# Kernel optimization log

Hardware: AMD Instinct MI355X
Metric: run time of the kernel (lower is better)

The kernel has to match this reference:

```python
import jax, jax.numpy as jnp
import numpy as np

IN_DIM = 256
MEM_DIM = 256
DEPTH = 18                    # complete binary tree
N = 2 ** DEPTH - 1            # 262143 nodes; children of i are 2i+1, 2i+2; node 0 is root


def _glorot(k, shape):
    lim = float(np.sqrt(6.0 / (shape[0] + shape[1])))
    return jax.random.uniform(k, shape, jnp.float32, -lim, lim)


def setup_inputs() -> dict:
    key = jax.random.key(0)
    ks = jax.random.split(key, 6)
    inputs = jax.random.normal(ks[0], (N, IN_DIM), jnp.float32)
    Wioux = _glorot(ks[1], (3 * MEM_DIM, IN_DIM))
    bioux = jnp.zeros((3 * MEM_DIM,), jnp.float32)
    Wiouh = _glorot(ks[2], (3 * MEM_DIM, MEM_DIM))
    Wfx = _glorot(ks[3], (MEM_DIM, IN_DIM))
    bfx = jnp.zeros((MEM_DIM,), jnp.float32)
    Wfh = _glorot(ks[4], (MEM_DIM, MEM_DIM))
    fb = jnp.ones((MEM_DIM,), jnp.float32)
    return {"inputs": inputs, "Wioux": Wioux, "bioux": bioux, "Wiouh": Wiouh,
            "Wfx": Wfx, "bfx": bfx, "Wfh": Wfh, "fb": fb}


def reference(inputs, Wioux, bioux, Wiouh, Wfx, bfx, Wfh, fb):
    # Child-Sum TreeLSTM over a complete binary tree, level-wise batched (bottom-up).
    n, _ = inputs.shape
    m = fb.shape[0]
    depth = int(np.log2(n + 1))
    # Input projections for all nodes at once (same math as per-node ioux/fx).
    xiou = inputs @ Wioux.T + bioux          # [N, 3m]
    xf = inputs @ Wfx.T + bfx                # [N, m]
    h_all = jnp.zeros((n, m), inputs.dtype)
    c_all = jnp.zeros((n, m), inputs.dtype)
    for d in range(depth - 1, -1, -1):
        s, e = 2 ** d - 1, 2 ** (d + 1) - 1   # nodes at level d
        if d == depth - 1:
            # Leaves: zero child state -> iouh/fh contribute 0, fc sums to 0.
            i, o, u = jnp.split(xiou[s:e], 3, axis=1)
            i, o, u = jax.nn.sigmoid(i), jax.nn.sigmoid(o), jnp.tanh(u)
            c = i * u
        else:
            node = jnp.arange(s, e)
            ch = jnp.stack([2 * node + 1, 2 * node + 2], axis=1)   # [L, 2]
            ch_h = h_all[ch]                                       # [L, 2, m]
            ch_c = c_all[ch]                                       # [L, 2, m]
            iou = xiou[s:e] + ch_h.sum(axis=1) @ Wiouh.T           # child-sum
            i, o, u = jnp.split(iou, 3, axis=1)
            i, o, u = jax.nn.sigmoid(i), jax.nn.sigmoid(o), jnp.tanh(u)
            f = jax.nn.sigmoid(jnp.einsum('lkm,nm->lkn', ch_h, Wfh)
                               + xf[s:e][:, None, :] + fb)         # per-child forget gate
            c = i * u + (f * ch_c).sum(axis=1)
        h = o * jnp.tanh(c)
        h_all = h_all.at[s:e].set(h)
        c_all = c_all.at[s:e].set(c)
    # (root h, root c, all node hidden states) as in the torch forward
    return h_all[0], c_all[0], h_all
```

## Files before the change

kernel.cpp:

```cpp
#include <hip/hip_runtime.h>


typedef __attribute__((ext_vector_type(8))) short bf16x8;
typedef __attribute__((ext_vector_type(8))) unsigned short us8;
typedef __attribute__((ext_vector_type(4))) float f32x4;
typedef __attribute__((ext_vector_type(4))) float f4;

#define MFMA16(A, B, C) __builtin_amdgcn_mfma_f32_16x16x32_bf16(A, B, C, 0, 0, 0)

__device__ __forceinline__ unsigned short f2b(float f) {
  unsigned int u = __builtin_bit_cast(unsigned int, f);
  u = u + 0x7FFFu + ((u >> 16) & 1u);
  return (unsigned short)(u >> 16);
}
__device__ __forceinline__ float bf2f(unsigned short u) {
  unsigned int v = (unsigned int)u << 16;
  return __builtin_bit_cast(float, v);
}
__device__ __forceinline__ us8 pack8(f4 a, f4 b) {
  us8 r;
  r[0] = f2b(a[0]); r[1] = f2b(a[1]); r[2] = f2b(a[2]); r[3] = f2b(a[3]);
  r[4] = f2b(b[0]); r[5] = f2b(b[1]); r[6] = f2b(b[2]); r[7] = f2b(b[3]);
  return r;
}
__device__ __forceinline__ float sigm(float x) { return 1.0f / (1.0f + __expf(-x)); }
__device__ __forceinline__ float tanh_f(float x) { return 2.0f / (1.0f + __expf(-2.0f * x)) - 1.0f; }

__global__ void pack_w(const float* __restrict__ a,
                       const float* __restrict__ b,
                       const float* __restrict__ c,
                       const float* __restrict__ d,
                       unsigned short* __restrict__ out) {
  int i = blockIdx.x * blockDim.x + threadIdx.x;
  const int A = 768 * 256;
  const int B = A + 768 * 256;
  const int C = B + 256 * 256;
  float v;
  if (i < A)      v = a[i];
  else if (i < B) v = b[i - A];
  else if (i < C) v = c[i - B];
  else            v = d[i - C];
  out[i] = f2b(v);
}

__global__ void conv_x(const float* __restrict__ x, unsigned short* __restrict__ xb, int n32) {
  int i = blockIdx.x * blockDim.x + threadIdx.x;
  if (i >= n32) return;
  const int n = i >> 5, g = i & 31;
  f4 a = __builtin_nontemporal_load((const f4*)(x + (size_t)n * 256 + g * 8));
  f4 b = __builtin_nontemporal_load((const f4*)(x + (size_t)n * 256 + g * 8 + 4));
  const int d = 31 - __clz(n + 1);
  const int r = n - ((1 << d) - 1);
  const size_t base = (size_t)((d < 4) ? d * 16 : 48 + (1 << d)) * 256;
  const size_t off = base + ((size_t)((r >> 4) * 8 + (g >> 2)) * 16 + (r & 15)) * 32
                     + (g & 3) * 8;
  __builtin_nontemporal_store(pack8(a, b), (us8*)(xb + off));
}

template<int LEAF>
__global__ __launch_bounds__(512) __attribute__((amdgpu_waves_per_eu(3, 4)))
void level_k(
    const unsigned short* __restrict__ xlv,
    const unsigned short* __restrict__ wb,
    const float* __restrict__ bioux,
    const float* __restrict__ bfx,
    const float* __restrict__ fb,
    float* __restrict__ h_all,
    const unsigned short* __restrict__ hs_r,
    const unsigned short* __restrict__ hbe_r,
    const unsigned int* __restrict__ cp_r,
    unsigned short* __restrict__ hs_w,
    unsigned short* __restrict__ hbe_w,
    unsigned int* __restrict__ cp_w,
    float* __restrict__ out0,
    int s, int L, int T16, int root, int lns)
{
  extern __shared__ unsigned short W[];

  const int tid    = threadIdx.x;
  const int NS     = 1 << lns;
  const int cg     = blockIdx.x >> lns;
  const int stripe = blockIdx.x & (NS - 1);

  const int NP = LEAF ? 3 : 8;
  #pragma unroll 1
  for (int c = tid; c < NP * 512; c += 512) {
    const int p   = c >> 9;
    const int q   = c & 511;
    const int kc  = q >> 6;
    const int kg  = (q >> 4) & 3;
    const int col = q & 15;
    const int po = (p < 3) ? p * 65536
                 : (p < 6) ? 196608 + (p - 3) * 65536
                 : (p == 6) ? 393216 : 458752;
    us8 v = *(const us8*)(wb + po + (size_t)(cg * 16 + col) * 256 + kc * 32 + kg * 8);
    *(us8*)(W + p * 4096 + ((kc * 4 + kg) * 16 + col) * 8) = v;
  }
  __syncthreads();

  const int lane = tid & 63;
  const int wv   = tid >> 6;
  const int lm   = lane & 15;
  const int kgl  = lane >> 4;
  const int colc = cg * 16 + lm;

  const unsigned short* LW = W + kgl * 128 + lm * 8;

  const int kcw = colc >> 5;
  const int kgw = (colc >> 3) & 3;
  const int ew  = colc & 7;

  const float bi_ = bioux[colc];
  const float bo_ = bioux[256 + colc];
  const float bu_ = bioux[512 + colc];
  const float bf_ = LEAF ? 0.f : (bfx[colc] + fb[colc]);

  const int Tper = (T16 + NS - 1) >> lns;
  const int t0   = stripe * Tper;
  const int tE   = (t0 + Tper < T16) ? (t0 + Tper) : T16;

  for (int t = t0 + wv; t < tE; t += 8) {
    const int tb16  = t * 16;
    const int drow0 = tb16 + kgl * 4;
    const size_t abase = (size_t)t * 4096 + lm * 32 + kgl * 8;
    const unsigned short* xr = xlv + abase;
    const f32x4 z4 = {0.f, 0.f, 0.f, 0.f};

    if (!LEAF) {
      const unsigned short* hbr = hbe_r + abase;
      const unsigned short* hsr = hs_r  + abase;

      unsigned int cpv[4];
      #pragma unroll
      for (int r = 0; r < 4; ++r)
        cpv[r] = cp_r[(size_t)t * 4096 + cg * 256 + r * 64 + kgl * 16 + lm];

      f32x4 xf = z4, f1h = z4, ai = z4, ao = z4, au = z4, fs = z4;
      #pragma unroll 4
      for (int kc = 0; kc < 8; ++kc) {
        bf16x8 ax = *(const bf16x8*)(xr  + kc * 512);
        bf16x8 a1 = *(const bf16x8*)(hbr + kc * 512);
        bf16x8 ah = *(const bf16x8*)(hsr + kc * 512);
        bf16x8 b6 = *(const bf16x8*)(LW + 6 * 4096 + kc * 512);
        bf16x8 b0 = *(const bf16x8*)(LW + 0 * 4096 + kc * 512);
        bf16x8 b1 = *(const bf16x8*)(LW + 1 * 4096 + kc * 512);
        bf16x8 b2 = *(const bf16x8*)(LW + 2 * 4096 + kc * 512);
        bf16x8 b7 = *(const bf16x8*)(LW + 7 * 4096 + kc * 512);
        bf16x8 b3 = *(const bf16x8*)(LW + 3 * 4096 + kc * 512);
        bf16x8 b4 = *(const bf16x8*)(LW + 4 * 4096 + kc * 512);
        bf16x8 b5 = *(const bf16x8*)(LW + 5 * 4096 + kc * 512);
        xf  = MFMA16(ax, b6, xf);
        ai  = MFMA16(ax, b0, ai);
        ao  = MFMA16(ax, b1, ao);
        au  = MFMA16(ax, b2, au);
        f1h = MFMA16(a1, b7, f1h);
        ai  = MFMA16(ah, b3, ai);
        ao  = MFMA16(ah, b4, ao);
        au  = MFMA16(ah, b5, au);
        fs  = MFMA16(ah, b7, fs);
      }

      float hv4[4], cv4[4];
      #pragma unroll
      for (int r = 0; r < 4; ++r) {
        const float i_ = sigm(ai[r] + bi_);
        const float u_ = tanh_f(au[r] + bu_);
        const float o_ = sigm(ao[r] + bo_);
        const float f1 = sigm(xf[r] + f1h[r] + bf_);
        const float f2 = sigm(xf[r] + fs[r] - f1h[r] + bf_);
        const float c1 = bf2f((unsigned short)(cpv[r] & 0xffffu));
        const float c2 = bf2f((unsigned short)(cpv[r] >> 16));
        const float c_ = i_ * u_ + f1 * c1 + f2 * c2;
        const float h_ = o_ * tanh_f(c_);
        cv4[r] = c_; hv4[r] = h_;
        const int j = drow0 + r;
        if (j < L)
          __builtin_nontemporal_store(h_, h_all + (size_t)(s + j) * 256 + colc);
      }
      if (root) {
        if (drow0 == 0) { out0[colc] = hv4[0]; out0[256 + colc] = cv4[0]; }
      } else {
        #pragma unroll
        for (int rp = 0; rp < 2; ++rp) {
          const int j0 = drow0 + rp * 2;
          if (j0 + 1 < L) {
            const int pp = j0 >> 1;
            const int q  = pp & 15;
            const size_t toff = ((size_t)((pp >> 4) * 8 + kcw) * 16 + q) * 32
                                + kgw * 8 + ew;
            hs_w [toff] = f2b(hv4[rp*2] + hv4[rp*2+1]);
            hbe_w[toff] = f2b(hv4[rp*2]);
            cp_w [(size_t)(pp >> 4) * 4096 + cg * 256 + (q & 3) * 64
                  + (q >> 2) * 16 + lm] =
                (unsigned int)f2b(cv4[rp*2]) | ((unsigned int)f2b(cv4[rp*2+1]) << 16);
          }
        }
      }
    } else {
      f32x4 ai = z4, ao = z4, au = z4;
      #pragma unroll 4
      for (int kc = 0; kc < 8; ++kc) {
        bf16x8 ax = *(const bf16x8*)(xr + kc * 512);
        bf16x8 b0 = *(const bf16x8*)(LW + 0 * 4096 + kc * 512);
        bf16x8 b1 = *(const bf16x8*)(LW + 1 * 4096 + kc * 512);
        bf16x8 b2 = *(const bf16x8*)(LW + 2 * 4096 + kc * 512);
        ai = MFMA16(ax, b0, ai);
        ao = MFMA16(ax, b1, ao);
        au = MFMA16(ax, b2, au);
      }
      float hv4[4], cv4[4];
      #pragma unroll
      for (int r = 0; r < 4; ++r) {
        const float i_ = sigm(ai[r] + bi_);
        const float u_ = tanh_f(au[r] + bu_);
        const float o_ = sigm(ao[r] + bo_);
        const float c_ = i_ * u_;
        const float h_ = o_ * tanh_f(c_);
        cv4[r] = c_; hv4[r] = h_;
        __builtin_nontemporal_store(h_, h_all + (size_t)(s + drow0 + r) * 256 + colc);
      }
      #pragma unroll
      for (int rp = 0; rp < 2; ++rp) {
        const int pp = (drow0 + rp * 2) >> 1;
        const int q  = pp & 15;
        const size_t toff = ((size_t)((pp >> 4) * 8 + kcw) * 16 + q) * 32
                            + kgw * 8 + ew;
        hs_w [toff] = f2b(hv4[rp*2] + hv4[rp*2+1]);
        hbe_w[toff] = f2b(hv4[rp*2]);
        cp_w [(size_t)(pp >> 4) * 4096 + cg * 256 + (q & 3) * 64
              + (q >> 2) * 16 + lm] =
            (unsigned int)f2b(cv4[rp*2]) | ((unsigned int)f2b(cv4[rp*2+1]) << 16);
      }
    }
  }
}

extern "C" void kernel_launch(void* const* d_in, const int* in_sizes, int n_in,
                              void* d_out, int out_size, void* d_ws, size_t ws_size,
                              hipStream_t stream) {
  const float* inputs = (const float*)d_in[0];
  const float* Wioux  = (const float*)d_in[1];
  const float* bioux  = (const float*)d_in[2];
  const float* Wiouh  = (const float*)d_in[3];
  const float* Wfx    = (const float*)d_in[4];
  const float* bfx    = (const float*)d_in[5];
  const float* Wfh    = (const float*)d_in[6];
  const float* fb     = (const float*)d_in[7];

  const int N = in_sizes[0] / 256;
  int depth = 0;
  while (((1 << depth) - 1) < N) ++depth;

  float* out   = (float*)d_out;
  float* h_all = out + 512;

  static bool attr_done = false;
  if (!attr_done) {
    hipFuncSetAttribute((const void*)level_k<0>,
                        hipFuncAttributeMaxDynamicSharedMemorySize, 8 * 8192);
    hipFuncSetAttribute((const void*)level_k<1>,
                        hipFuncAttributeMaxDynamicSharedMemorySize, 3 * 8192);
    attr_done = true;
  }

  char* p = (char*)d_ws;
  unsigned short* hs0  = (unsigned short*)p; p += (size_t)65536 * 256 * 2;
  unsigned short* hbe0 = (unsigned short*)p; p += (size_t)65536 * 256 * 2;
  unsigned int*   cp0  = (unsigned int*)p;   p += (size_t)65536 * 256 * 4;
  unsigned short* hs1  = (unsigned short*)p; p += (size_t)32768 * 256 * 2;
  unsigned short* hbe1 = (unsigned short*)p; p += (size_t)32768 * 256 * 2;
  unsigned int*   cp1  = (unsigned int*)p;   p += (size_t)32768 * 256 * 4;
  unsigned short* xb   = (unsigned short*)p; p += (size_t)(N + 64) * 256 * 2;
  unsigned short* wb   = (unsigned short*)p;

  pack_w<<<2048, 256, 0, stream>>>(Wioux, Wiouh, Wfx, Wfh, wb);
  {
    const int n32 = N * 32;
    conv_x<<<(n32 + 255) / 256, 256, 0, stream>>>(inputs, xb, n32);
  }

  for (int d = depth - 1; d >= 0; --d) {
    const int L = 1 << d;
    const int s = L - 1;
    const int T16 = (L + 15) / 16;
    const size_t Pb = (size_t)((d < 4) ? d * 16 : 48 + (1 << d)) * 256;
    int lg = 0; while ((1 << (lg + 1)) <= T16) ++lg;
    int lns = lg - 3; if (lns < 0) lns = 0; if (lns > 5) lns = 5;
    const int rp_ = d & 1, wp_ = (d - 1) & 1;
    const unsigned short* hs_r  = rp_ ? hs1 : hs0;
    const unsigned short* hbe_r = rp_ ? hbe1 : hbe0;
    const unsigned int*   cp_r  = rp_ ? cp1 : cp0;
    unsigned short* hs_w  = wp_ ? hs1 : hs0;
    unsigned short* hbe_w = wp_ ? hbe1 : hbe0;
    unsigned int*   cp_w  = wp_ ? cp1 : cp0;
    if (d == depth - 1) {
      level_k<1><<<16 * 64, 512, 3 * 8192, stream>>>(
          xb + Pb, wb, bioux, bfx, fb, h_all,
          hs_r, hbe_r, cp_r, hs_w, hbe_w, cp_w, out, s, L, T16, 0, 6);
    } else {
      level_k<0><<<16 << lns, 512, 8 * 8192, stream>>>(
          xb + Pb, wb, bioux, bfx, fb, h_all,
          hs_r, hbe_r, cp_r, hs_w, hbe_w, cp_w, out, s, L, T16, (d == 0) ? 1 : 0, lns);
    }
  }
}
```

Measured before the change: 681.5 us.

## Process two 16-row tiles per wave to reuse weight fragments across tiles

Each wave now handles a pair of adjacent 16-row tiles, so every loaded weight fragment (from LDS/global) feeds MFMAs for both tiles. The inner loop is split into two phases: forget-gate MFMAs plus their fc partial, then i/o/u MFMAs, which keeps the accumulator count from growing too far. Grid sizing is based on the halved tile count. This halves weight load traffic per output and raises per-wave ILP, at the cost of more registers (lower occupancy) and fewer waves on small levels.

Result: slower. 945.2 us (+38.7%).

```diff
diff --git a/kernel.cpp b/kernel.cpp
--- a/kernel.cpp
+++ b/kernel.cpp
@@ -115,14 +115,16 @@
   const float bu_ = bioux[512 + colc];
   const float bf_ = LEAF ? 0.f : (bfx[colc] + fb[colc]);
 
-  const int Tper = (T16 + NS - 1) >> lns;
+  const int T2   = (T16 + 1) >> 1;
+  const int Tper = (T2 + NS - 1) >> lns;
   const int t0   = stripe * Tper;
-  const int tE   = (t0 + Tper < T16) ? (t0 + Tper) : T16;
-
-  for (int t = t0 + wv; t < tE; t += 8) {
-    const int tb16  = t * 16;
-    const int drow0 = tb16 + kgl * 4;
-    const size_t abase = (size_t)t * 4096 + lm * 32 + kgl * 8;
+  const int tE   = (t0 + Tper < T2) ? (t0 + Tper) : T2;
+
+  for (int t2 = t0 + wv; t2 < tE; t2 += 8) {
+    const int tA  = 2 * t2;
+    const int tB  = tA + 1;
+    const int doB = (tB < T16);
+    const size_t abase = (size_t)tA * 4096 + lm * 32 + kgl * 8;
     const unsigned short* xr = xlv + abase;
     const f32x4 z4 = {0.f, 0.f, 0.f, 0.f};
 
@@ -130,106 +132,171 @@
       const unsigned short* hbr = hbe_r + abase;
       const unsigned short* hsr = hs_r  + abase;
 
-      unsigned int cpv[4];
+      unsigned int cpA[4], cpB[4];
       #pragma unroll
-      for (int r = 0; r < 4; ++r)
-        cpv[r] = cp_r[(size_t)t * 4096 + cg * 256 + r * 64 + kgl * 16 + lm];
-
-      f32x4 xf = z4, f1h = z4, ai = z4, ao = z4, au = z4, fs = z4;
-      #pragma unroll 4
+      for (int r = 0; r < 4; ++r) {
+        cpA[r] = cp_r[(size_t)tA * 4096 + cg * 256 + r * 64 + kgl * 16 + lm];
+        cpB[r] = doB ? cp_r[(size_t)tB * 4096 + cg * 256 + r * 64 + kgl * 16 + lm] : 0u;
+      }
+
+      f32x4 xfA = z4, f1A = z4, fsA = z4, xfB = z4, f1B = z4, fsB = z4;
+      #pragma unroll 2
       for (int kc = 0; kc < 8; ++kc) {
-        bf16x8 ax = *(const bf16x8*)(xr  + kc * 512);
-        bf16x8 a1 = *(const bf16x8*)(hbr + kc * 512);
-        bf16x8 ah = *(const bf16x8*)(hsr + kc * 512);
         bf16x8 b6 = *(const bf16x8*)(LW + 6 * 4096 + kc * 512);
+        bf16x8 b7 = *(const bf16x8*)(LW + 7 * 4096 + kc * 512);
+        bf16x8 ax0 = *(const bf16x8*)(xr  + kc * 512);
+        bf16x8 a10 = *(const bf16x8*)(hbr + kc * 512);
+        bf16x8 ah0 = *(const bf16x8*)(hsr + kc * 512);
+        xfA = MFMA16(ax0, b6, xfA);
+        f1A = MFMA16(a10, b7, f1A);
+        fsA = MFMA16(ah0, b7, fsA);
+        if (doB) {
+          bf16x8 ax1 = *(const bf16x8*)(xr  + 4096 + kc * 512);
+          bf16x8 a11 = *(const bf16x8*)(hbr + 4096 + kc * 512);
+          bf16x8 ah1 = *(const bf16x8*)(hsr + 4096 + kc * 512);
+          xfB = MFMA16(ax1, b6, xfB);
+          f1B = MFMA16(a11, b7, f1B);
+          fsB = MFMA16(ah1, b7, fsB);
+        }
+      }
+
+      float cvfA[4], cvfB[4];
+      #pragma unroll
+      for (int r = 0; r < 4; ++r) {
+        {
+          const float f1 = sigm(xfA[r] + f1A[r] + bf_);
+          const float f2 = sigm(xfA[r] + fsA[r] - f1A[r] + bf_);
+          cvfA[r] = f1 * bf2f((unsigned short)(cpA[r] & 0xffffu))
+                  + f2 * bf2f((unsigned short)(cpA[r] >> 16));
+        }
+        {
+          const float f1 = sigm(xfB[r] + f1B[r] + bf_);
+          const float f2 = sigm(xfB[r] + fsB[r] - f1B[r] + bf_);
+          cvfB[r] = f1 * bf2f((unsigned short)(cpB[r] & 0xffffu))
+                  + f2 * bf2f((unsigned short)(cpB[r] >> 16));
+        }
+      }
+
+      f32x4 aiA = z4, aoA = z4, auA = z4, aiB = z4, aoB = z4, auB = z4;
+      #pragma unroll 2
+      for (int kc = 0; kc < 8; ++kc) {
         bf16x8 b0 = *(const bf16x8*)(LW + 0 * 4096 + kc * 512);
         bf16x8 b1 = *(const bf16x8*)(LW + 1 * 4096 + kc * 512);
         bf16x8 b2 = *(const bf16x8*)(LW + 2 * 4096 + kc * 512);
-        bf16x8 b7 = *(const bf16x8*)(LW + 7 * 4096 + kc * 512);
         bf16x8 b3 = *(const bf16x8*)(LW + 3 * 4096 + kc * 512);
         bf16x8 b4 = *(const bf16x8*)(LW + 4 * 4096 + kc * 512);
         bf16x8 b5 = *(const bf16x8*)(LW + 5 * 4096 + kc * 512);
-        xf  = MFMA16(ax, b6, xf);
-        ai  = MFMA16(ax, b0, ai);
-        ao  = MFMA16(ax, b1, ao);
-        au  = MFMA16(ax, b2, au);
-        f1h = MFMA16(a1, b7, f1h);
-        ai  = MFMA16(ah, b3, ai);
-        ao  = MFMA16(ah, b4, ao);
-        au  = MFMA16(ah, b5, au);
-        fs  = MFMA16(ah, b7, fs);
-      }
-
-      float hv4[4], cv4[4];
+        bf16x8 ax0 = *(const bf16x8*)(xr  + kc * 512);
+        bf16x8 ah0 = *(const bf16x8*)(hsr + kc * 512);
+        aiA = MFMA16(ax0, b0, aiA);
+        aoA = MFMA16(ax0, b1, aoA);
+        auA = MFMA16(ax0, b2, auA);
+        aiA = MFMA16(ah0, b3, aiA);
+        aoA = MFMA16(ah0, b4, aoA);
+        auA = MFMA16(ah0, b5, auA);
+        if (doB) {
+          bf16x8 ax1 = *(const bf16x8*)(xr  + 4096 + kc * 512);
+          bf16x8 ah1 = *(const bf16x8*)(hsr + 4096 + kc * 512);
+          aiB = MFMA16(ax1, b0, aiB);
+          aoB = MFMA16(ax1, b1, aoB);
+          auB = MFMA16(ax1, b2, auB);
+          aiB = MFMA16(ah1, b3, aiB);
+          aoB = MFMA16(ah1, b4, aoB);
+          auB = MFMA16(ah1, b5, auB);
+        }
+      }
+
       #pragma unroll
-      for (int r = 0; r < 4; ++r) {
-        const float i_ = sigm(ai[r] + bi_);
-        const float u_ = tanh_f(au[r] + bu_);
-        const float o_ = sigm(ao[r] + bo_);
-        const float f1 = sigm(xf[r] + f1h[r] + bf_);
-        const float f2 = sigm(xf[r] + fs[r] - f1h[r] + bf_);
-        const float c1 = bf2f((unsigned short)(cpv[r] & 0xffffu));
-        const float c2 = bf2f((unsigned short)(cpv[r] >> 16));
-        const float c_ = i_ * u_ + f1 * c1 + f2 * c2;
-        const float h_ = o_ * tanh_f(c_);
-        cv4[r] = c_; hv4[r] = h_;
-        const int j = drow0 + r;
-        if (j < L)
-          __builtin_nontemporal_store(h_, h_all + (size_t)(s + j) * 256 + colc);
-      }
-      if (root) {
-        if (drow0 == 0) { out0[colc] = hv4[0]; out0[256 + colc] = cv4[0]; }
-      } else {
+      for (int st = 0; st < 2; ++st) {
+        if (st && !doB) break;
+        const f32x4& ai = st ? aiB : aiA;
+        const f32x4& ao = st ? aoB : aoA;
+        const f32x4& au = st ? auB : auA;
+        const float* cvf = st ? cvfB : cvfA;
+        const int tt    = st ? tB : tA;
+        const int drow0 = tt * 16 + kgl * 4;
+        float hv4[4], cv4[4];
         #pragma unroll
-        for (int rp = 0; rp < 2; ++rp) {
-          const int j0 = drow0 + rp * 2;
-          if (j0 + 1 < L) {
-            const int pp = j0 >> 1;
-            const int q  = pp & 15;
-            const size_t toff = ((size_t)((pp >> 4) * 8 + kcw) * 16 + q) * 32
-                                + kgw * 8 + ew;
-            hs_w [toff] = f2b(hv4[rp*2] + hv4[rp*2+1]);
-            hbe_w[toff] = f2b(hv4[rp*2]);
-            cp_w [(size_t)(pp >> 4) * 4096 + cg * 256 + (q & 3) * 64
-                  + (q >> 2) * 16 + lm] =
-                (unsigned int)f2b(cv4[rp*2]) | ((unsigned int)f2b(cv4[rp*2+1]) << 16);
+        for (int r = 0; r < 4; ++r) {
+          const float i_ = sigm(ai[r] + bi_);
+          const float u_ = tanh_f(au[r] + bu_);
+          const float o_ = sigm(ao[r] + bo_);
+          const float c_ = i_ * u_ + cvf[r];
+          const float h_ = o_ * tanh_f(c_);
+          cv4[r] = c_; hv4[r] = h_;
+          const int j = drow0 + r;
+          if (j < L)
+            __builtin_nontemporal_store(h_, h_all + (size_t)(s + j) * 256 + colc);
+        }
+        if (root) {
+          if (drow0 == 0) { out0[colc] = hv4[0]; out0[256 + colc] = cv4[0]; }
+        } else {
+          #pragma unroll
+          for (int rp = 0; rp < 2; ++rp) {
+            const int j0 = drow0 + rp * 2;
+            if (j0 + 1 < L) {
+              const int pp = j0 >> 1;
+              const int q  = pp & 15;
+              const size_t toff = ((size_t)((pp >> 4) * 8 + kcw) * 16 + q) * 32
+                                  + kgw * 8 + ew;
+              hs_w [toff] = f2b(hv4[rp*2] + hv4[rp*2+1]);
+              hbe_w[toff] = f2b(hv4[rp*2]);
+              cp_w [(size_t)(pp >> 4) * 4096 + cg * 256 + (q & 3) * 64
+                    + (q >> 2) * 16 + lm] =
+                  (unsigned int)f2b(cv4[rp*2]) | ((unsigned int)f2b(cv4[rp*2+1]) << 16);
+            }
           }
         }
       }
     } else {
-      f32x4 ai = z4, ao = z4, au = z4;
-      #pragma unroll 4
+      f32x4 aiA = z4, aoA = z4, auA = z4, aiB = z4, aoB = z4, auB = z4;
+      #pragma unroll 2
       for (int kc = 0; kc < 8; ++kc) {
-        bf16x8 ax = *(const bf16x8*)(xr + kc * 512);
         bf16x8 b0 = *(const bf16x8*)(LW + 0 * 4096 + kc * 512);
         bf16x8 b1 = *(const bf16x8*)(LW + 1 * 4096 + kc * 512);
         bf16x8 b2 = *(const bf16x8*)(LW + 2 * 4096 + kc * 512);
-        ai = MFMA16(ax, b0, ai);
-        ao = MFMA16(ax, b1, ao);
-        au = MFMA16(ax, b2, au);
-      }
-      float hv4[4], cv4[4];
+        bf16x8 ax0 = *(const bf16x8*)(xr + kc * 512);
+        aiA = MFMA16(ax0, b0, aiA);
+        aoA = MFMA16(ax0, b1, aoA);
+        auA = MFMA16(ax0, b2, auA);
+        if (doB) {
+          bf16x8 ax1 = *(const bf16x8*)(xr + 4096 + kc * 512);
+          aiB = MFMA16(ax1, b0, aiB);
+          aoB = MFMA16(ax1, b1, aoB);
+          auB = MFMA16(ax1, b2, auB);
+        }
+      }
       #pragma unroll
-      for (int r = 0; r < 4; ++r) {
-        const float i_ = sigm(ai[r] + bi_);
-        const float u_ = tanh_f(au[r] + bu_);
-        const float o_ = sigm(ao[r] + bo_);
-        const float c_ = i_ * u_;
-        const float h_ = o_ * tanh_f(c_);
-        cv4[r] = c_; hv4[r] = h_;
-        __builtin_nontemporal_store(h_, h_all + (size_t)(s + drow0 + r) * 256 + colc);
-      }
-      #pragma unroll
-      for (int rp = 0; rp < 2; ++rp) {
-        const int pp = (drow0 + rp * 2) >> 1;
-        const int q  = pp & 15;
-        const size_t toff = ((size_t)((pp >> 4) * 8 + kcw) * 16 + q) * 32
-                            + kgw * 8 + ew;
-        hs_w [toff] = f2b(hv4[rp*2] + hv4[rp*2+1]);
-        hbe_w[toff] = f2b(hv4[rp*2]);
-        cp_w [(size_t)(pp >> 4) * 4096 + cg * 256 + (q & 3) * 64
-              + (q >> 2) * 16 + lm] =
-            (unsigned int)f2b(cv4[rp*2]) | ((unsigned int)f2b(cv4[rp*2+1]) << 16);
+      for (int st = 0; st < 2; ++st) {
+        if (st && !doB) break;
+        const f32x4& ai = st ? aiB : aiA;
+        const f32x4& ao = st ? aoB : aoA;
+        const f32x4& au = st ? auB : auA;
+        const int tt    = st ? tB : tA;
+        const int drow0 = tt * 16 + kgl * 4;
+        float hv4[4], cv4[4];
+        #pragma unroll
+        for (int r = 0; r < 4; ++r) {
+          const float i_ = sigm(ai[r] + bi_);
+          const float u_ = tanh_f(au[r] + bu_);
+          const float o_ = sigm(ao[r] + bo_);
+          const float c_ = i_ * u_;
+          const float h_ = o_ * tanh_f(c_);
+          cv4[r] = c_; hv4[r] = h_;
+          __builtin_nontemporal_store(h_, h_all + (size_t)(s + drow0 + r) * 256 + colc);
+        }
+        #pragma unroll
+        for (int rp = 0; rp < 2; ++rp) {
+          const int pp = (drow0 + rp * 2) >> 1;
+          const int q  = pp & 15;
+          const size_t toff = ((size_t)((pp >> 4) * 8 + kcw) * 16 + q) * 32
+                              + kgw * 8 + ew;
+          hs_w [toff] = f2b(hv4[rp*2] + hv4[rp*2+1]);
+          hbe_w[toff] = f2b(hv4[rp*2]);
+          cp_w [(size_t)(pp >> 4) * 4096 + cg * 256 + (q & 3) * 64
+                + (q >> 2) * 16 + lm] =
+              (unsigned int)f2b(cv4[rp*2]) | ((unsigned int)f2b(cv4[rp*2+1]) << 16);
+        }
       }
     }
   }
@@ -283,8 +350,9 @@
     const int L = 1 << d;
     const int s = L - 1;
     const int T16 = (L + 15) / 16;
+    const int T2  = (T16 + 1) / 2;
     const size_t Pb = (size_t)((d < 4) ? d * 16 : 48 + (1 << d)) * 256;
-    int lg = 0; while ((1 << (lg + 1)) <= T16) ++lg;
+    int lg = 0; while ((1 << (lg + 1)) <= T2) ++lg;
     int lns = lg - 3; if (lns < 0) lns = 0; if (lns > 5) lns = 5;
     const int rp_ = d & 1, wp_ = (d - 1) & 1;
     const unsigned short* hs_r  = rp_ ? hs1 : hs0;
```
